# Kernel optimization log

Hardware: AMD Instinct MI355X
Metric: run time of the kernel (lower is better)

The kernel has to match this reference:

```python
import jax, jax.numpy as jnp
import numpy as np

B, N, IN_F, OUT_F = 32, 1024, 256, 256


def setup_inputs() -> dict:
    key = jax.random.key(0)
    k_adj, k_feat, k_w, k_b = jax.random.split(key, 4)
    adjacency = jax.random.uniform(k_adj, (B, N, N), dtype=jnp.float32)  # [B,N,N]
    features = jax.random.normal(k_feat, (B, N, IN_F), dtype=jnp.float32)  # [B,N,in]
    # 'thomas' init ~ uniform(-1/sqrt(fan_in), 1/sqrt(fan_in)) style; scale is
    # irrelevant to correctness-checking, use scaled normal.
    weight = jax.random.normal(k_w, (IN_F, OUT_F), dtype=jnp.float32) / np.sqrt(IN_F)
    bias = jax.random.normal(k_b, (OUT_F,), dtype=jnp.float32) / np.sqrt(IN_F)
    return {"adjacency": adjacency, "features": features, "weight": weight, "bias": bias}


def reference(adjacency, features, weight, bias) -> jnp.ndarray:
    # support = features @ weight : [B,N,out]
    support = jnp.einsum("bni,io->bno", features, weight)
    # output = bmm(adjacency, support) : [B,N,out]
    output = jnp.einsum("bnm,bmo->bno", adjacency, support)
    return output + bias
```

## Files before the change

### kernel.cpp

```cpp
#include <hip/hip_runtime.h>
#include <hip/hip_bf16.h>


typedef __attribute__((__ext_vector_type__(4))) float  f32x4;
typedef __attribute__((__ext_vector_type__(8))) __bf16 bf16x8;
typedef __attribute__((__ext_vector_type__(4))) __bf16 bf16x4;

#define BK 64

__device__ __forceinline__ void gld16(const void* g, void* l) {
  __builtin_amdgcn_global_load_lds(
      (const __attribute__((address_space(1))) unsigned int*)g,
      (__attribute__((address_space(3))) unsigned int*)l, 16, 0, 0);
}

__global__ __launch_bounds__(256) void k_wt(const float* __restrict__ w,
                                            __bf16* __restrict__ Wt) {
  __shared__ __bf16 T[64][65];
  const int bi = blockIdx.x >> 2;
  const int bj = blockIdx.x & 3;
  const int t  = threadIdx.x;
  const int r  = t >> 2;
  const int q  = t & 3;
  const float* src = w + (size_t)(bi * 64 + r) * 256 + bj * 64 + q * 16;
#pragma unroll
  for (int u = 0; u < 4; ++u) {
    f32x4 v = *(const f32x4*)(src + u * 4);
    T[r][q * 16 + u * 4 + 0] = (__bf16)v[0];
    T[r][q * 16 + u * 4 + 1] = (__bf16)v[1];
    T[r][q * 16 + u * 4 + 2] = (__bf16)v[2];
    T[r][q * 16 + u * 4 + 3] = (__bf16)v[3];
  }
  __syncthreads();
  bf16x8 h0, h1;
#pragma unroll
  for (int u = 0; u < 8; ++u) {
    h0[u] = T[q * 16 + u][r];
    h1[u] = T[q * 16 + 8 + u][r];
  }
  __bf16* d0 = Wt + ((size_t)(bi * 8 + q * 2) * 256 + (bj * 64 + r)) * 8;
  *(bf16x8*)d0          = h0;
  *(bf16x8*)(d0 + 2048) = h1;
}

template <int KTOT, int LDA, bool EPI_ST>
__global__ __launch_bounds__(512, 2) void k_gemm(
    const float* __restrict__ Aall, const __bf16* __restrict__ Bg_all,
    const float* __restrict__ bias, float* __restrict__ Out,
    __bf16* __restrict__ St) {
  __shared__ float  Af[2][128 * 64];
  __shared__ __bf16 Bf[2][8 * 256 * 8];

  const int tid  = threadIdx.x;
  const int lane = tid & 63;
  const int wid  = tid >> 6;
  const int wr   = wid >> 2;
  const int wc   = wid & 3;
  const int l16  = lane & 15;
  const int g    = lane >> 4;

  int b, mblk;
  const float*  Ablk;
  const __bf16* Bblk;
  if constexpr (EPI_ST) {
    const int bx = blockIdx.x;
    b    = bx >> 3;
    mblk = bx & 7;
    Ablk = Aall + (size_t)bx * 128 * LDA;
    Bblk = Bg_all;
  } else {
    const int h  = blockIdx.x;
    const int lg = (h & 7) * 32 + (h >> 3);
    b    = lg >> 3;
    mblk = lg & 7;
    Ablk = Aall + (size_t)b * 1024 * 1024 + (size_t)mblk * 128 * LDA;
    Bblk = Bg_all + (size_t)b * 262144;
  }

  const float*  aS[4];
  const __bf16* bS[4];
#pragma unroll
  for (int i = 0; i < 4; ++i) {
    const int c = i * 512 + tid;
    aS[i] = Ablk + (size_t)(c >> 4) * LDA + (((c & 15) ^ ((c >> 4) & 7)) << 2);
    bS[i] = Bblk + (size_t)c * 8;
  }

#define STAGE(buf, k0)                                                        \
  {                                                                           \
    const size_t koff = (size_t)((k0) >> 3) * 2048;                           \
    _Pragma("unroll") for (int i = 0; i < 4; ++i) {                           \
      gld16(aS[i] + (k0), &Af[buf][(i * 512 + wid * 64) * 4]);                \
      gld16(bS[i] + koff, &Bf[buf][(i * 512 + wid * 64) * 8]);                \
    }                                                                         \
  }

  f32x4 acc[4][4];
#pragma unroll
  for (int m = 0; m < 4; ++m)
#pragma unroll
    for (int n = 0; n < 4; ++n) acc[m][n] = (f32x4){0.f, 0.f, 0.f, 0.f};

  auto compute = [&](int buf) {
#pragma unroll
    for (int ks = 0; ks < 2; ++ks) {
      bf16x8 af[4], bv[4];
#pragma unroll
      for (int m = 0; m < 4; ++m) {
        const int row = wr * 64 + m * 16 + l16;
        const int rx  = row & 7;
        const int c0  = (ks * 8 + 2 * g) ^ rx;
        const int c1  = (ks * 8 + 2 * g + 1) ^ rx;
        f32x4 v0 = *(const f32x4*)&Af[buf][row * 64 + c0 * 4];
        f32x4 v1 = *(const f32x4*)&Af[buf][row * 64 + c1 * 4];
        af[m] = (bf16x8){(__bf16)v0[0], (__bf16)v0[1], (__bf16)v0[2], (__bf16)v0[3],
                         (__bf16)v1[0], (__bf16)v1[1], (__bf16)v1[2], (__bf16)v1[3]};
      }
#pragma unroll
      for (int n = 0; n < 4; ++n) {
        const int col = wc * 64 + n * 16 + l16;
        bv[n] = *(const bf16x8*)&Bf[buf][((ks * 4 + g) * 256 + col) * 8];
      }
#pragma unroll
      for (int m = 0; m < 4; ++m)
#pragma unroll
        for (int n = 0; n < 4; ++n)
          acc[m][n] = __builtin_amdgcn_mfma_f32_16x16x32_bf16(af[m], bv[n], acc[m][n], 0, 0, 0);
    }
  };

  constexpr int NT = KTOT / BK;
  STAGE(0, 0);
  __syncthreads();
  for (int t = 0; t < NT - 2; t += 2) {
    STAGE(1, (t + 1) * BK);
    compute(0);
    __syncthreads();
    STAGE(0, (t + 2) * BK);
    compute(1);
    __syncthreads();
  }
  STAGE(1, (NT - 1) * BK);
  compute(0);
  __syncthreads();
  compute(1);
#undef STAGE

  const int rg = g * 4;
  if constexpr (EPI_ST) {
    __bf16* Stb = St + (size_t)b * 262144;
    const int gm0 = mblk * 128 + wr * 64;
#pragma unroll
    for (int n = 0; n < 4; ++n) {
      const int col = wc * 64 + n * 16 + l16;
#pragma unroll
      for (int m = 0; m < 4; ++m) {
        const int gm = gm0 + m * 16 + rg;
        __bf16* dst = Stb + (size_t)(gm >> 3) * 2048 + (size_t)col * 8 + (gm & 7);
        bf16x4 hh = {(__bf16)acc[m][n][0], (__bf16)acc[m][n][1],
                     (__bf16)acc[m][n][2], (__bf16)acc[m][n][3]};
        *(bf16x4*)dst = hh;
      }
    }
  } else {
    float* ob = Out + ((size_t)b * 1024 + (size_t)mblk * 128 + wr * 64) * 256;
#pragma unroll
    for (int n = 0; n < 4; ++n) {
      const int col = wc * 64 + n * 16 + l16;
      const float bvs = bias[col];
#pragma unroll
      for (int m = 0; m < 4; ++m) {
        const int row = m * 16 + rg;
#pragma unroll
        for (int r2 = 0; r2 < 4; ++r2)
          ob[(size_t)(row + r2) * 256 + col] = acc[m][n][r2] + bvs;
      }
    }
  }
}

extern "C" void kernel_launch(void* const* d_in, const int* in_sizes, int n_in,
                              void* d_out, int out_size, void* d_ws, size_t ws_size,
                              hipStream_t stream) {
  const float* adj  = (const float*)d_in[0];
  const float* feat = (const float*)d_in[1];
  const float* w    = (const float*)d_in[2];
  const float* bias = (const float*)d_in[3];
  float* out = (float*)d_out;

  __bf16* Wt = (__bf16*)d_ws;
  __bf16* St = (__bf16*)((char*)d_ws + 131072);

  k_wt<<<16, 256, 0, stream>>>(w, Wt);
  k_gemm<256, 256, true><<<256, 512, 0, stream>>>(feat, Wt, nullptr, nullptr, St);
  k_gemm<1024, 1024, false><<<256, 512, 0, stream>>>(adj, St, bias, out, nullptr);
}
```

Measured before the change: 54.09 us.

## Stage A tiles through registers as bf16 in LDS with prefetch two ahead

The fp32 A operand is no longer copied straight into LDS with global_load_lds and converted on every fragment read. Each thread now loads fp32 into registers two k-tiles ahead, converts once to bf16 and writes a swizzled bf16 tile to LDS. This halves LDS footprint and read traffic for A and removes repeated conversions in the inner loop, and MFMA sections get raised wave priority via setprio. The cost is more VGPRs for the two register staging buffers, which could hurt occupancy at 512 threads with launch bounds of 2 blocks, plus explicit VMEM waits before the LDS writes.

```diff
diff --git a/kernel.cpp b/kernel.cpp
--- a/kernel.cpp
+++ b/kernel.cpp
@@ -48,7 +48,7 @@
     const float* __restrict__ Aall, const __bf16* __restrict__ Bg_all,
     const float* __restrict__ bias, float* __restrict__ Out,
     __bf16* __restrict__ St) {
-  __shared__ float  Af[2][128 * 64];
+  __shared__ __bf16 Af[2][128 * 64];
   __shared__ __bf16 Bf[2][8 * 256 * 8];
 
   const int tid  = threadIdx.x;
@@ -77,23 +77,40 @@
     Bblk = Bg_all + (size_t)b * 262144;
   }
 
-  const float*  aS[4];
+  const int    srow = tid >> 2;
+  const int    sq   = tid & 3;
+  const float* asrc = Ablk + (size_t)srow * LDA + sq * 16;
+  const int wof0 = srow * 64 + (((sq * 2)     ^ (srow & 7)) << 3);
+  const int wof1 = srow * 64 + (((sq * 2 + 1) ^ (srow & 7)) << 3);
+
   const __bf16* bS[4];
 #pragma unroll
-  for (int i = 0; i < 4; ++i) {
-    const int c = i * 512 + tid;
-    aS[i] = Ablk + (size_t)(c >> 4) * LDA + (((c & 15) ^ ((c >> 4) & 7)) << 2);
-    bS[i] = Bblk + (size_t)c * 8;
-  }
-
-#define STAGE(buf, k0)                                                        \
+  for (int i = 0; i < 4; ++i) bS[i] = Bblk + (size_t)(i * 512 + tid) * 8;
+
+#define LOADA(S, k0)                                                          \
+  {                                                                           \
+    _Pragma("unroll") for (int u = 0; u < 4; ++u)                             \
+        S[u] = *(const f32x4*)(asrc + (k0) + u * 4);                          \
+  }
+#define ISSUEB(buf, k0)                                                       \
   {                                                                           \
     const size_t koff = (size_t)((k0) >> 3) * 2048;                           \
-    _Pragma("unroll") for (int i = 0; i < 4; ++i) {                           \
-      gld16(aS[i] + (k0), &Af[buf][(i * 512 + wid * 64) * 4]);                \
-      gld16(bS[i] + koff, &Bf[buf][(i * 512 + wid * 64) * 8]);                \
-    }                                                                         \
-  }
+    _Pragma("unroll") for (int i = 0; i < 4; ++i)                             \
+        gld16(bS[i] + koff, &Bf[buf][(i * 512 + wid * 64) * 8]);              \
+  }
+#define CVTW(S, buf)                                                          \
+  {                                                                           \
+    bf16x8 h0 = {(__bf16)S[0][0], (__bf16)S[0][1], (__bf16)S[0][2],           \
+                 (__bf16)S[0][3], (__bf16)S[1][0], (__bf16)S[1][1],           \
+                 (__bf16)S[1][2], (__bf16)S[1][3]};                           \
+    bf16x8 h1 = {(__bf16)S[2][0], (__bf16)S[2][1], (__bf16)S[2][2],           \
+                 (__bf16)S[2][3], (__bf16)S[3][0], (__bf16)S[3][1],           \
+                 (__bf16)S[3][2], (__bf16)S[3][3]};                           \
+    *(bf16x8*)&Af[buf][wof0] = h0;                                            \
+    *(bf16x8*)&Af[buf][wof1] = h1;                                            \
+  }
+
+  f32x4 S0[4], S1[4];
 
   f32x4 acc[4][4];
 #pragma unroll
@@ -107,44 +124,53 @@
       bf16x8 af[4], bv[4];
 #pragma unroll
       for (int m = 0; m < 4; ++m) {
-        const int row = wr * 64 + m * 16 + l16;
-        const int rx  = row & 7;
-        const int c0  = (ks * 8 + 2 * g) ^ rx;
-        const int c1  = (ks * 8 + 2 * g + 1) ^ rx;
-        f32x4 v0 = *(const f32x4*)&Af[buf][row * 64 + c0 * 4];
-        f32x4 v1 = *(const f32x4*)&Af[buf][row * 64 + c1 * 4];
-        af[m] = (bf16x8){(__bf16)v0[0], (__bf16)v0[1], (__bf16)v0[2], (__bf16)v0[3],
-                         (__bf16)v1[0], (__bf16)v1[1], (__bf16)v1[2], (__bf16)v1[3]};
+        const int row  = wr * 64 + m * 16 + l16;
+        const int slot = (ks * 4 + g) ^ (row & 7);
+        af[m] = *(const bf16x8*)&Af[buf][row * 64 + slot * 8];
       }
 #pragma unroll
       for (int n = 0; n < 4; ++n) {
         const int col = wc * 64 + n * 16 + l16;
         bv[n] = *(const bf16x8*)&Bf[buf][((ks * 4 + g) * 256 + col) * 8];
       }
+      __builtin_amdgcn_s_setprio(1);
 #pragma unroll
       for (int m = 0; m < 4; ++m)
 #pragma unroll
         for (int n = 0; n < 4; ++n)
           acc[m][n] = __builtin_amdgcn_mfma_f32_16x16x32_bf16(af[m], bv[n], acc[m][n], 0, 0, 0);
+      __builtin_amdgcn_s_setprio(0);
     }
   };
 
   constexpr int NT = KTOT / BK;
-  STAGE(0, 0);
+  LOADA(S0, 0);
+  ISSUEB(0, 0);
+  LOADA(S1, BK);
+  CVTW(S0, 0);
   __syncthreads();
+
   for (int t = 0; t < NT - 2; t += 2) {
-    STAGE(1, (t + 1) * BK);
+    LOADA(S0, (t + 2) * BK);
+    ISSUEB(1, (t + 1) * BK);
     compute(0);
+    CVTW(S1, 1);
     __syncthreads();
-    STAGE(0, (t + 2) * BK);
+    LOADA(S1, (t + 3) * BK);
+    ISSUEB(0, (t + 2) * BK);
     compute(1);
+    CVTW(S0, 0);
     __syncthreads();
   }
-  STAGE(1, (NT - 1) * BK);
+  ISSUEB(1, (NT - 1) * BK);
   compute(0);
+  CVTW(S1, 1);
   __syncthreads();
   compute(1);
-#undef STAGE
+
+#undef LOADA
+#undef ISSUEB
+#undef CVTW
 
   const int rg = g * 4;
   if constexpr (EPI_ST) {
```

After: 53.07 us. Within noise of the previous version (-1.9%).
